# Kernel tuning notes

Hardware: AMD Instinct MI355X
Metric: run time of the kernel (lower is better)

## Reference

```python
import jax, jax.numpy as jnp
import numpy as np

C, H, W = 128, 376, 1248
N = 200000

def setup_inputs() -> dict:
    key = jax.random.key(0)
    k1, k2, k3 = jax.random.split(key, 3)
    feature_map = jax.random.normal(k1, (C, H, W), dtype=jnp.float32)
    # u in [0, W-2), v in [0, H-2) so that floor+1 stays in-bounds
    u = jax.random.uniform(k2, (N,), dtype=jnp.float32) * (W - 2)
    v = jax.random.uniform(k3, (N,), dtype=jnp.float32) * (H - 2)
    target_uv = jnp.stack([u, v], axis=1)  # [N, 2]
    return {"feature_map": feature_map, "target_uv": target_uv, "downscale": 1}

def reference(feature_map, target_uv, downscale):
    # feature_map: [C, H, W], target_uv: [N, 2] (u, v)
    u = target_uv[:, 0] / downscale
    v = target_uv[:, 1] / downscale
    u_lo = u.astype(jnp.int32)
    v_lo = v.astype(jnp.int32)
    u_hi = u_lo + 1
    v_hi = v_lo + 1
    du = u - u_lo.astype(jnp.float32)
    dv = v - v_lo.astype(jnp.float32)
    # Four gathers [C, N] + bilinear blend
    out = (feature_map[:, v_lo, u_lo] * ((1 - dv) * (1 - du))
           + feature_map[:, v_hi, u_lo] * (dv * (1 - du))
           + feature_map[:, v_lo, u_hi] * ((1 - dv) * du)
           + feature_map[:, v_hi, u_hi] * (dv * du))
    return out  # [C, N]
```

## Files before the change

### kernel.cpp

```cpp
#include <hip/hip_runtime.h>
#include <hip/hip_fp16.h>

constexpr int C = 128, H = 376, W = 1248;
constexpr int HW = H * W;

constexpr int BIN  = 14;
constexpr int BU   = (W + BIN - 1) / BIN;
constexpr int BV   = (H + BIN - 1) / BIN;
constexpr int NBINS = BU * BV;
constexpr int CAP  = 160;
constexpr int CPG  = 16;
constexpr int NCG  = C / CPG;
constexpr int ROWS = BIN + 1;
constexpr int CHROW = 4;
constexpr int RWF  = CHROW * 4;
constexpr int CH_CHUNKS = ROWS * CHROW + 1;
constexpr int CH_F = CH_CHUNKS * 4;
constexpr int BLK_CHUNKS = CPG * CH_CHUNKS;
constexpr int STG = (BLK_CHUNKS + 255) / 256;

typedef float vfloat4 __attribute__((ext_vector_type(4)));

__global__ __launch_bounds__(512) void k0_init(int* cursor) {
    for (int i = threadIdx.x + blockIdx.x * 512; i < NBINS; i += gridDim.x * 512)
        cursor[i] = i * CAP;
}

__global__ __launch_bounds__(256) void k3_scatter(const float* __restrict__ uv,
                                                  const int* __restrict__ dsp,
                                                  int* __restrict__ cursor,
                                                  uint4* __restrict__ sorted,
                                                  int* __restrict__ inv, int N) {
    int n = blockIdx.x * 256 + threadIdx.x;
    if (n >= N) return;
    float dsf = (float)dsp[0];
    float2 p = ((const float2*)uv)[n];
    float u = p.x / dsf, v = p.y / dsf;
    int ul = (int)u, vl = (int)v;
    float du = u - (float)ul, dv = v - (float)vl;
    int bin = (vl / BIN) * BU + (ul / BIN);
    int pos = atomicAdd(cursor + bin, 1);
    uint4 rec;
    rec.x = (unsigned)(ul | (vl << 16));
    rec.y = __float_as_uint(du);
    rec.z = __float_as_uint(dv);
    rec.w = (unsigned)n;
    sorted[pos] = rec;
    inv[n] = pos;
}

__global__ __launch_bounds__(256) void k4_resample(const float* __restrict__ fmap,
                                                   const uint4* __restrict__ sorted,
                                                   const int* __restrict__ cursor,
                                                   __half* __restrict__ mid, int N) {
    __shared__ float lds[BLK_CHUNKS * 4];

    int bin = blockIdx.x >> 3;
    int cg  = blockIdx.x & 7;
    int bu  = bin % BU;
    int bv  = bin / BU;
    int u0  = bu * BIN;
    int v0  = bv * BIN;
    int cb  = cg * CPG;
    int tid = threadIdx.x;

    vfloat4 stg[STG];
#pragma unroll
    for (int i = 0; i < STG; ++i) {
        int k = tid + i * 256;
        if (k < BLK_CHUNKS) {
            int ch   = k / CH_CHUNKS;
            int rem  = k - ch * CH_CHUNKS;
            int rem2 = min(rem, ROWS * CHROW - 1);
            int r    = rem2 / CHROW;
            int c4   = rem2 - r * CHROW;
            int gr   = min(v0 + r, H - 1);
            int gc   = min(u0 + c4 * 4, W - 4);
            stg[i] = *(const vfloat4*)(fmap + (size_t)(cb + ch) * HW + (size_t)gr * W + gc);
        }
    }
    __builtin_amdgcn_sched_barrier(0);
#pragma unroll
    for (int i = 0; i < STG; ++i) {
        int k = tid + i * 256;
        if (k < BLK_CHUNKS)
            *(vfloat4*)&lds[k * 4] = stg[i];
    }
    __syncthreads();

    int s = bin * CAP, e = cursor[bin];
    int q = tid & 3;
    const float* chbase = &lds[q * 4 * CH_F];
    __half* midbase = mid + ((size_t)cg * (size_t)NBINS * CAP) * 16 + q * 4;
    for (int p = s + (tid >> 2); p < e; p += 64) {
        uint4 pt = sorted[p];
        int ul = (int)(pt.x & 0xffffu);
        int vl = (int)(pt.x >> 16);
        float du = __uint_as_float(pt.y);
        float dv = __uint_as_float(pt.z);

        float w00 = (1.0f - dv) * (1.0f - du);
        float w10 = dv * (1.0f - du);
        float w01 = (1.0f - dv) * du;
        float w11 = dv * du;

        const float* base = chbase + (vl - v0) * RWF + (ul - u0);
        float r[4];
#pragma unroll
        for (int c = 0; c < 4; ++c) {
            float f00 = base[c * CH_F];
            float f01 = base[c * CH_F + 1];
            float f10 = base[c * CH_F + RWF];
            float f11 = base[c * CH_F + RWF + 1];
            r[c] = f00 * w00 + f10 * w10 + f01 * w01 + f11 * w11;
        }
        union { __half2 h2[2]; uint2 u; } pk;
        pk.h2[0] = __floats2half2_rn(r[0], r[1]);
        pk.h2[1] = __floats2half2_rn(r[2], r[3]);
        *(uint2*)(midbase + (size_t)p * 16) = pk.u;
    }
}

__global__ __launch_bounds__(256) void k5_permute(const __half* __restrict__ mid,
                                                  const int* __restrict__ inv,
                                                  float* __restrict__ out, int N) {
    __shared__ float tile[64 * 132];
    __shared__ int   sp[64];
    int n0 = blockIdx.x * 64;
    int t  = threadIdx.x;
    int cnt = min(64, N - n0);

    if (t < 64) sp[t] = (t < cnt) ? inv[n0 + t] : 0;
    __syncthreads();

    int j  = t >> 2;
    int q4 = t & 3;
    constexpr size_t CGSTRIDE = (size_t)NBINS * CAP;
    uint2 g[8];
#pragma unroll
    for (int r = 0; r < 8; ++r) {
        if (j < cnt)
            g[r] = *(const uint2*)(mid + ((size_t)r * CGSTRIDE + sp[j]) * 16 + q4 * 4);
    }
#pragma unroll
    for (int r = 0; r < 8; ++r) {
        if (j < cnt) {
            union { uint2 u; __half2 h2[2]; } pk; pk.u = g[r];
            float2 f0 = __half22float2(pk.h2[0]);
            float2 f1 = __half22float2(pk.h2[1]);
            vfloat4 w = {f0.x, f0.y, f1.x, f1.y};
            *(vfloat4*)&tile[j * 132 + r * 16 + q4 * 4] = w;
        }
    }
    __syncthreads();

    int jj = t & 63;
    for (int s = 0; s < 32; ++s) {
        int c = s * 4 + (t >> 6);
        if (jj < cnt)
            __builtin_nontemporal_store(tile[jj * 132 + c], out + (size_t)c * N + n0 + jj);
    }
}

constexpr int F_CPG = 2;
constexpr int F_CG  = C / F_CPG;
constexpr int F_GPX = F_CG / 8;

__global__ __launch_bounds__(256) void fallback_kernel(
    const float* __restrict__ fmap, const float* __restrict__ uv,
    const int* __restrict__ dsp, float* __restrict__ out, int N, int NBX)
{
    int bid = blockIdx.x;
    int xcd = bid & 7;
    int jj  = bid >> 3;
    int g_local = jj / NBX;
    int nb      = jj - g_local * NBX;
    int g   = xcd * F_GPX + g_local;

    int n = nb * 256 + threadIdx.x;
    if (n >= N) return;

    float dsf = (float)dsp[0];
    float2 p = ((const float2*)uv)[n];
    float u = p.x / dsf, v = p.y / dsf;
    int u_lo = (int)u, v_lo = (int)v;
    float du = u - (float)u_lo, dv = v - (float)v_lo;

    float w00 = (1.0f - dv) * (1.0f - du);
    float w10 = dv * (1.0f - du);
    float w01 = (1.0f - dv) * du;
    float w11 = dv * du;

    int cbase = g * F_CPG;
    const float* fp = fmap + (size_t)cbase * HW + (size_t)v_lo * W + u_lo;
    float*       op = out  + (size_t)cbase * N + n;
#pragma unroll
    for (int c = 0; c < F_CPG; ++c) {
        float f00 = fp[0], f01 = fp[1], f10 = fp[W], f11 = fp[W + 1];
        float r = f00 * w00 + f10 * w10 + f01 * w01 + f11 * w11;
        __builtin_nontemporal_store(r, op);
        fp += HW; op += N;
    }
}

extern "C" void kernel_launch(void* const* d_in, const int* in_sizes, int n_in,
                              void* d_out, int out_size, void* d_ws, size_t ws_size,
                              hipStream_t stream)
{
    const float* fmap = (const float*)d_in[0];
    const float* uv   = (const float*)d_in[1];
    const int*   dsp  = (const int*)d_in[2];
    float*       out  = (float*)d_out;

    int N = in_sizes[1] / 2;

    size_t off_cursor = 0;
    size_t off_inv    = 16384;
    size_t off_sorted = off_inv + (((size_t)N * 4 + 255) & ~(size_t)255);
    size_t off_mid    = off_sorted + (((size_t)NBINS * CAP * 16 + 255) & ~(size_t)255);
    size_t need       = off_mid + (size_t)NBINS * CAP * 32 * NCG;

    if (ws_size < need) {
        int NBX = (N + 255) / 256;
        dim3 grid(NBX * F_CG);
        fallback_kernel<<<grid, dim3(256), 0, stream>>>(fmap, uv, dsp, out, N, NBX);
        return;
    }

    char* ws = (char*)d_ws;
    int*    cursor = (int*)(ws + off_cursor);
    int*    inv    = (int*)(ws + off_inv);
    uint4*  sorted = (uint4*)(ws + off_sorted);
    __half* mid    = (__half*)(ws + off_mid);

    int nb = (N + 255) / 256;
    k0_init<<<4, 512, 0, stream>>>(cursor);
    k3_scatter<<<nb, 256, 0, stream>>>(uv, dsp, cursor, sorted, inv, N);
    k4_resample<<<NBINS * NCG, 256, 0, stream>>>(fmap, sorted, cursor, mid, N);
    k5_permute<<<(N + 63) / 64, 256, 0, stream>>>(mid, inv, out, N);
}
```

Measured before the change: 155.8 us.

## Pack sort records to 8 bytes with 16-bit fractions; shrink resample blocks

Sort records drop the unused point index and store du/dv as 16-bit fixed-point, so each record shrinks from 16 to 8 bytes. This halves scatter write and resample read traffic for the records. The resample kernel also drops from 256 to 192 threads per block, which changes staging iterations and occupancy, and the bin cursor read moves before the staging loads. Quantising the interpolation weights to 16 bits adds error on the order of 1e-5 on top of the existing fp16 intermediate.

```diff
diff --git a/kernel.cpp b/kernel.cpp
--- a/kernel.cpp
+++ b/kernel.cpp
@@ -17,7 +17,8 @@
 constexpr int CH_CHUNKS = ROWS * CHROW + 1;
 constexpr int CH_F = CH_CHUNKS * 4;
 constexpr int BLK_CHUNKS = CPG * CH_CHUNKS;
-constexpr int STG = (BLK_CHUNKS + 255) / 256;
+constexpr int K4T  = 192;
+constexpr int STG = (BLK_CHUNKS + K4T - 1) / K4T;
 
 typedef float vfloat4 __attribute__((ext_vector_type(4)));
 
@@ -29,7 +30,7 @@
 __global__ __launch_bounds__(256) void k3_scatter(const float* __restrict__ uv,
                                                   const int* __restrict__ dsp,
                                                   int* __restrict__ cursor,
-                                                  uint4* __restrict__ sorted,
+                                                  uint2* __restrict__ sorted,
                                                   int* __restrict__ inv, int N) {
     int n = blockIdx.x * 256 + threadIdx.x;
     if (n >= N) return;
@@ -40,17 +41,15 @@
     float du = u - (float)ul, dv = v - (float)vl;
     int bin = (vl / BIN) * BU + (ul / BIN);
     int pos = atomicAdd(cursor + bin, 1);
-    uint4 rec;
+    uint2 rec;
     rec.x = (unsigned)(ul | (vl << 16));
-    rec.y = __float_as_uint(du);
-    rec.z = __float_as_uint(dv);
-    rec.w = (unsigned)n;
+    rec.y = (unsigned)(du * 65535.f + 0.5f) | ((unsigned)(dv * 65535.f + 0.5f) << 16);
     sorted[pos] = rec;
     inv[n] = pos;
 }
 
-__global__ __launch_bounds__(256) void k4_resample(const float* __restrict__ fmap,
-                                                   const uint4* __restrict__ sorted,
+__global__ __launch_bounds__(K4T) void k4_resample(const float* __restrict__ fmap,
+                                                   const uint2* __restrict__ sorted,
                                                    const int* __restrict__ cursor,
                                                    __half* __restrict__ mid, int N) {
     __shared__ float lds[BLK_CHUNKS * 4];
@@ -63,11 +62,13 @@
     int v0  = bv * BIN;
     int cb  = cg * CPG;
     int tid = threadIdx.x;
+    int s   = bin * CAP;
+    int e   = cursor[bin];
 
     vfloat4 stg[STG];
 #pragma unroll
     for (int i = 0; i < STG; ++i) {
-        int k = tid + i * 256;
+        int k = tid + i * K4T;
         if (k < BLK_CHUNKS) {
             int ch   = k / CH_CHUNKS;
             int rem  = k - ch * CH_CHUNKS;
@@ -82,22 +83,21 @@
     __builtin_amdgcn_sched_barrier(0);
 #pragma unroll
     for (int i = 0; i < STG; ++i) {
-        int k = tid + i * 256;
+        int k = tid + i * K4T;
         if (k < BLK_CHUNKS)
             *(vfloat4*)&lds[k * 4] = stg[i];
     }
     __syncthreads();
 
-    int s = bin * CAP, e = cursor[bin];
     int q = tid & 3;
     const float* chbase = &lds[q * 4 * CH_F];
     __half* midbase = mid + ((size_t)cg * (size_t)NBINS * CAP) * 16 + q * 4;
-    for (int p = s + (tid >> 2); p < e; p += 64) {
-        uint4 pt = sorted[p];
+    for (int p = s + (tid >> 2); p < e; p += (K4T / 4)) {
+        uint2 pt = sorted[p];
         int ul = (int)(pt.x & 0xffffu);
         int vl = (int)(pt.x >> 16);
-        float du = __uint_as_float(pt.y);
-        float dv = __uint_as_float(pt.z);
+        float du = (float)(pt.y & 0xffffu) * (1.0f / 65535.0f);
+        float dv = (float)(pt.y >> 16)     * (1.0f / 65535.0f);
 
         float w00 = (1.0f - dv) * (1.0f - du);
         float w10 = dv * (1.0f - du);
@@ -217,7 +217,7 @@
     size_t off_cursor = 0;
     size_t off_inv    = 16384;
     size_t off_sorted = off_inv + (((size_t)N * 4 + 255) & ~(size_t)255);
-    size_t off_mid    = off_sorted + (((size_t)NBINS * CAP * 16 + 255) & ~(size_t)255);
+    size_t off_mid    = off_sorted + (((size_t)NBINS * CAP * 8 + 255) & ~(size_t)255);
     size_t need       = off_mid + (size_t)NBINS * CAP * 32 * NCG;
 
     if (ws_size < need) {
@@ -230,12 +230,12 @@
     char* ws = (char*)d_ws;
     int*    cursor = (int*)(ws + off_cursor);
     int*    inv    = (int*)(ws + off_inv);
-    uint4*  sorted = (uint4*)(ws + off_sorted);
+    uint2*  sorted = (uint2*)(ws + off_sorted);
     __half* mid    = (__half*)(ws + off_mid);
 
     int nb = (N + 255) / 256;
     k0_init<<<4, 512, 0, stream>>>(cursor);
     k3_scatter<<<nb, 256, 0, stream>>>(uv, dsp, cursor, sorted, inv, N);
-    k4_resample<<<NBINS * NCG, 256, 0, stream>>>(fmap, sorted, cursor, mid, N);
+    k4_resample<<<NBINS * NCG, K4T, 0, stream>>>(fmap, sorted, cursor, mid, N);
     k5_permute<<<(N + 63) / 64, 256, 0, stream>>>(mid, inv, out, N);
 }
```

New measurement: 184.0 us. 18.1% more time.
